# Optimization experiments

Hardware: AMD Instinct MI355X
Metric: run time of the kernel (lower is better)

The kernel has to match this reference:

```python
import jax, jax.numpy as jnp
import numpy as np


def setup_inputs() -> dict:
    key = jax.random.key(0)
    ks = jax.random.split(key, 7)
    B, D, H, M, E = 8192, 512, 512, 50, 3
    return {
        "x": jax.random.normal(ks[0], (B, D), dtype=jnp.float32),
        "mem": jax.random.normal(ks[1], (M, D), dtype=jnp.float32),
        "routing_logits": jax.random.normal(ks[2], (E,), dtype=jnp.float32),
        "proj_W": jax.random.normal(ks[3], (H, D), dtype=jnp.float32) * 0.02,
        "proj_b": jax.random.normal(ks[4], (H,), dtype=jnp.float32) * 0.02,
        "ops_W": jax.random.normal(ks[5], (E, H, H), dtype=jnp.float32) * 0.02,
        "ops_b": jax.random.normal(ks[6], (E, H), dtype=jnp.float32) * 0.02,
    }


def reference(x, mem, routing_logits, proj_W, proj_b, ops_W, ops_b):
    # novelty: mean over (batch, memory) of L2 distance between x rows and memory rows
    diff = x[:, None, :] - mem[None, :, :]                 # [B, M, D] -- dominant memory traffic
    novelty = jnp.minimum(1.5, jnp.mean(jnp.linalg.norm(diff, axis=-1)))

    # top-2 routing over softmax of the (per-module, input-independent) logits
    weights = jax.nn.softmax(routing_logits)
    _, top2 = jax.lax.top_k(weights, 2)
    idx_a, idx_b = top2[0], top2[1]

    # operator = ReLU -> Linear(H, H) -> ReLU (torch Linear: y = x @ W.T + b)
    def op(h, W, b):
        return jax.nn.relu(jnp.einsum("bh,oh->bo", jax.nn.relu(h), W) + b)

    x_proj = jnp.einsum("bd,hd->bh", x, proj_W) + proj_b   # [B, H]
    x1 = op(x_proj, ops_W[idx_a], ops_b[idx_a])
    out = op(x1, ops_W[idx_b], ops_b[idx_b])
    return out, novelty
```

## Files before the change

kernel.cpp:

```cpp
#include <hip/hip_runtime.h>
#include <hip/hip_bf16.h>

typedef _Float16 f16;
typedef _Float16 f16x8 __attribute__((ext_vector_type(8)));
typedef float f32x4 __attribute__((ext_vector_type(4)));

#define BD 512

__device__ __forceinline__ void llds16(const f16* g, f16* l) {
  __builtin_amdgcn_global_load_lds(
      (const __attribute__((address_space(1))) unsigned int*)g,
      (__attribute__((address_space(3))) unsigned int*)l,
      16, 0, 0);
}

__global__ __launch_bounds__(256) void conv_nov_w_kernel(
    const float* __restrict__ x, const float* __restrict__ memf,
    const float* __restrict__ projW, const float* __restrict__ opsW,
    f16* __restrict__ wh, f16* __restrict__ xh,
    float* __restrict__ novPart) {
  __shared__ __align__(16) f16 As[16 * BD];
  __shared__ float xn[16];
  __shared__ float red[4];
  const int t = threadIdx.x, l = t & 63, w = t >> 6;
  const int rbase = blockIdx.x * 16;

  {
    const int e = (blockIdx.x * 256 + t) * 8;
    const float* s = (e < 262144) ? (projW + e) : (opsW + (e - 262144));
    float4 v0 = ((const float4*)s)[0];
    float4 v1 = ((const float4*)s)[1];
    f16x8 h;
    h[0]=(f16)v0.x; h[1]=(f16)v0.y; h[2]=(f16)v0.z; h[3]=(f16)v0.w;
    h[4]=(f16)v1.x; h[5]=(f16)v1.y; h[6]=(f16)v1.z; h[7]=(f16)v1.w;
    *(f16x8*)&wh[e] = h;
  }

  #pragma unroll
  for (int rr = 0; rr < 4; ++rr) {
    const int r = w * 4 + rr;
    const float* src = x + (size_t)(rbase + r) * BD + l * 8;
    float4 v0 = *(const float4*)src;
    float4 v1 = *(const float4*)(src + 4);
    f16x8 h;
    h[0]=(f16)v0.x; h[1]=(f16)v0.y; h[2]=(f16)v0.z; h[3]=(f16)v0.w;
    h[4]=(f16)v1.x; h[5]=(f16)v1.y; h[6]=(f16)v1.z; h[7]=(f16)v1.w;
    *(f16x8*)&xh[(size_t)(rbase + r) * BD + l * 8] = h;
    const int cs = l ^ (r & 7);
    *(f16x8*)&As[r * BD + cs * 8] = h;
    float ss = v0.x*v0.x + v0.y*v0.y + v0.z*v0.z + v0.w*v0.w
             + v1.x*v1.x + v1.y*v1.y + v1.z*v1.z + v1.w*v1.w;
    #pragma unroll
    for (int off = 32; off; off >>= 1) ss += __shfl_down(ss, off, 64);
    if (l == 0) xn[r] = ss;
  }
  __syncthreads();

  const int lr = l & 15, lk = l >> 4;
  if (w < 4) {
    const int mm = w * 16 + lr;
    f32x4 acc = (f32x4){0.f, 0.f, 0.f, 0.f};
    float msq = 0.f;
    #pragma unroll
    for (int kk = 0; kk < BD; kk += 32) {
      f16x8 bfr;
      if (mm < 50) {
        const float* ms = memf + (size_t)mm * BD + kk + lk * 8;
        float4 v0 = ((const float4*)ms)[0];
        float4 v1 = ((const float4*)ms)[1];
        bfr[0]=(f16)v0.x; bfr[1]=(f16)v0.y; bfr[2]=(f16)v0.z; bfr[3]=(f16)v0.w;
        bfr[4]=(f16)v1.x; bfr[5]=(f16)v1.y; bfr[6]=(f16)v1.z; bfr[7]=(f16)v1.w;
        msq += v0.x*v0.x + v0.y*v0.y + v0.z*v0.z + v0.w*v0.w
             + v1.x*v1.x + v1.y*v1.y + v1.z*v1.z + v1.w*v1.w;
      } else {
        #pragma unroll
        for (int j = 0; j < 8; ++j) bfr[j] = (f16)0.f;
      }
      const int ch = (kk >> 3) + lk;
      f16x8 a = *(const f16x8*)&As[lr * BD + ((ch ^ (lr & 7)) << 3)];
      acc = __builtin_amdgcn_mfma_f32_16x16x32_f16(a, bfr, acc, 0, 0, 0);
    }
    msq += __shfl_xor(msq, 16, 64);
    msq += __shfl_xor(msq, 32, 64);
    float local = 0.f;
    if (mm < 50) {
      #pragma unroll
      for (int j = 0; j < 4; ++j) {
        const int r0 = lk * 4 + j;
        float d = xn[r0] - 2.f * acc[j] + msq;
        local += sqrtf(fmaxf(d, 0.f));
      }
    }
    #pragma unroll
    for (int off = 32; off; off >>= 1) local += __shfl_down(local, off, 64);
    if (l == 0) red[w] = local;
  }
  __syncthreads();
  if (t == 0) novPart[blockIdx.x] = red[0] + red[1] + red[2] + red[3];
}

template <int PICK, int OUTF16>
__global__ __launch_bounds__(256, 3) void gemm_relu_kernel(
    const f16* __restrict__ A, const f16* __restrict__ Wall,
    const float* __restrict__ ball, const float* __restrict__ logits,
    void* __restrict__ Out, const float* __restrict__ novPart,
    float* __restrict__ novOut) {
  __shared__ __align__(16) char lds[3 * 16384];

  const int t = threadIdx.x;
  const int l = t & 63;
  const int w = t >> 6;
  const int wr = w >> 1, wc = w & 1;
  const int lr = l & 15, lk = l >> 4;

  if (PICK == 0 && blockIdx.x == 0 && blockIdx.y == 0 && w == 0) {
    float s = 0.f;
    #pragma unroll
    for (int i = 0; i < 8; ++i) s += novPart[l + i * 64];
    #pragma unroll
    for (int off = 32; off; off >>= 1) s += __shfl_down(s, off, 64);
    if (l == 0) novOut[0] = fminf(1.5f, s * (1.0f / (8192.0f * 50.0f)));
  }

  int widx = 0;
  if (PICK > 0) {
    float l0 = logits[0], l1 = logits[1], l2 = logits[2];
    int ia = 0; float ba = l0;
    if (l1 > ba) { ba = l1; ia = 1; }
    if (l2 > ba) { ba = l2; ia = 2; }
    if (PICK == 1) {
      widx = ia;
    } else {
      int ib = 0; float bb2 = -3.4e38f;
      if (ia != 0)             { bb2 = l0; ib = 0; }
      if (ia != 1 && l1 > bb2) { bb2 = l1; ib = 1; }
      if (ia != 2 && l2 > bb2) { bb2 = l2; ib = 2; }
      widx = ib;
    }
  }
  const f16* W = Wall + (size_t)widx * BD * BD;
  const float* bias = ball + widx * BD;

  const int rowBase = blockIdx.x * 64;
  const int colBase = blockIdx.y * 64;

  f32x4 acc[2][2];
  #pragma unroll
  for (int m = 0; m < 2; ++m)
    #pragma unroll
    for (int n = 0; n < 2; ++n) acc[m][n] = (f32x4){0.f, 0.f, 0.f, 0.f};

  auto stage = [&](int buf, int kt) {
    f16* Ab = (f16*)(lds + buf * 16384);
    f16* Bb = (f16*)(lds + buf * 16384 + 8192);
    #pragma unroll
    for (int i = 0; i < 2; ++i) {
      const int o = i * 4096 + t * 16;
      const int row = o >> 7;
      const int sch = ((o >> 4) & 7) ^ (row & 7);
      llds16(A + (size_t)(rowBase + row) * BD + kt + sch * 8,
             Ab + (i * 4096 + w * 1024) / 2);
      llds16(W + (size_t)(colBase + row) * BD + kt + sch * 8,
             Bb + (i * 4096 + w * 1024) / 2);
    }
  };

  auto compute = [&](int buf) {
    const f16* Ab = (const f16*)(lds + buf * 16384);
    const f16* Bb = (const f16*)(lds + buf * 16384 + 8192);
    #pragma unroll
    for (int kk = 0; kk < 64; kk += 32) {
      const int ch = (kk >> 3) + lk;
      f16x8 af[2], bf[2];
      #pragma unroll
      for (int m = 0; m < 2; ++m) {
        const int row = wr * 32 + m * 16 + lr;
        af[m] = *(const f16x8*)&Ab[row * 64 + ((ch ^ (row & 7)) << 3)];
      }
      #pragma unroll
      for (int n = 0; n < 2; ++n) {
        const int row = wc * 32 + n * 16 + lr;
        bf[n] = *(const f16x8*)&Bb[row * 64 + ((ch ^ (row & 7)) << 3)];
      }
      __builtin_amdgcn_s_setprio(1);
      #pragma unroll
      for (int m = 0; m < 2; ++m)
        #pragma unroll
        for (int n = 0; n < 2; ++n)
          acc[m][n] = __builtin_amdgcn_mfma_f32_16x16x32_f16(af[m], bf[n], acc[m][n], 0, 0, 0);
      __builtin_amdgcn_s_setprio(0);
    }
  };

  stage(0, 0);
  stage(1, 64);
  #pragma unroll
  for (int t8 = 0; t8 < 8; ++t8) {
    if (t8 < 7) asm volatile("s_waitcnt vmcnt(4)" ::: "memory");
    else        asm volatile("s_waitcnt vmcnt(0)" ::: "memory");
    __builtin_amdgcn_s_barrier();
    if (t8 < 6) stage((t8 + 2) % 3, (t8 + 2) * 64);
    compute(t8 % 3);
    asm volatile("s_waitcnt lgkmcnt(0)" ::: "memory");
  }

  #pragma unroll
  for (int n = 0; n < 2; ++n) {
    const int col = colBase + wc * 32 + n * 16 + lr;
    const float bbv = bias[col];
    #pragma unroll
    for (int m = 0; m < 2; ++m) {
      #pragma unroll
      for (int j = 0; j < 4; ++j) {
        const int rowg = rowBase + wr * 32 + m * 16 + lk * 4 + j;
        float v = fmaxf(acc[m][n][j] + bbv, 0.f);
        if (OUTF16) ((f16*)Out)[(size_t)rowg * BD + col] = (f16)v;
        else        ((float*)Out)[(size_t)rowg * BD + col] = v;
      }
    }
  }
}

extern "C" void kernel_launch(void* const* d_in, const int* in_sizes, int n_in,
                              void* d_out, int out_size, void* d_ws, size_t ws_size,
                              hipStream_t stream) {
  const float* x      = (const float*)d_in[0];
  const float* memf   = (const float*)d_in[1];
  const float* logits = (const float*)d_in[2];
  const float* projW  = (const float*)d_in[3];
  const float* projB  = (const float*)d_in[4];
  const float* opsW   = (const float*)d_in[5];
  const float* opsB   = (const float*)d_in[6];
  float* out = (float*)d_out;

  char* ws = (char*)d_ws;
  f16*   xh      = (f16*)(ws);
  f16*   g0      = (f16*)(ws + 8388608);
  f16*   wh      = (f16*)(ws + 16777216);
  float* novPart = (float*)(ws + 18874368);

  conv_nov_w_kernel<<<512, 256, 0, stream>>>(x, memf, projW, opsW, wh, xh, novPart);

  gemm_relu_kernel<0, 1><<<dim3(128, 8), 256, 0, stream>>>(
      xh, wh, projB, logits, (void*)g0, novPart, out + 4194304);
  gemm_relu_kernel<1, 1><<<dim3(128, 8), 256, 0, stream>>>(
      g0, wh + 262144, opsB, logits, (void*)xh, novPart, out + 4194304);
  gemm_relu_kernel<2, 0><<<dim3(128, 8), 256, 0, stream>>>(
      xh, wh + 262144, opsB, logits, (void*)out, novPart, out + 4194304);
}
```

Measured before the change: 47.02 us.

## Stage memory rows in LDS as f16 and deepen GEMM pipeline to four buffers

The novelty kernel now loads all 50 memory rows once per block into LDS as swizzled f16, replacing per-wave global fp32 loads and conversions inside the K loop. The squared norm of each memory row is now computed from the f16 values, which slightly changes precision. The GEMM kernels move from a three-buffer to a four-buffer LDS ring, with three stages in flight and adjusted vmcnt waits, so that global-load latency is better hidden. In exchange, the larger LDS footprint (64KB per GEMM block, about 68KB for the novelty kernel) lowers occupancy bounds to 2 blocks per CU.

```diff
diff --git a/kernel.cpp b/kernel.cpp
--- a/kernel.cpp
+++ b/kernel.cpp
@@ -2,6 +2,7 @@
 #include <hip/hip_bf16.h>
 
 typedef _Float16 f16;
+typedef _Float16 f16x4 __attribute__((ext_vector_type(4)));
 typedef _Float16 f16x8 __attribute__((ext_vector_type(8)));
 typedef float f32x4 __attribute__((ext_vector_type(4)));
 
@@ -14,16 +15,29 @@
       16, 0, 0);
 }
 
-__global__ __launch_bounds__(256) void conv_nov_w_kernel(
+__global__ __launch_bounds__(256, 2) void conv_nov_w_kernel(
     const float* __restrict__ x, const float* __restrict__ memf,
     const float* __restrict__ projW, const float* __restrict__ opsW,
     f16* __restrict__ wh, f16* __restrict__ xh,
     float* __restrict__ novPart) {
+  __shared__ __align__(16) f16 memh[52 * BD];
   __shared__ __align__(16) f16 As[16 * BD];
   __shared__ float xn[16];
   __shared__ float red[4];
   const int t = threadIdx.x, l = t & 63, w = t >> 6;
   const int rbase = blockIdx.x * 16;
+
+  #pragma unroll
+  for (int i = 0; i < 25; ++i) {
+    const int idx = i * 256 + t;
+    const int row = idx >> 7;
+    const int c4  = idx & 127;
+    float4 v = ((const float4*)memf)[(size_t)row * 128 + c4];
+    f16x4 h;
+    h[0]=(f16)v.x; h[1]=(f16)v.y; h[2]=(f16)v.z; h[3]=(f16)v.w;
+    const int ch = c4 >> 1;
+    *(f16x4*)&memh[row * BD + (((ch ^ (row & 7)) << 3) | ((c4 & 1) << 2))] = h;
+  }
 
   {
     const int e = (blockIdx.x * 256 + t) * 8;
@@ -59,31 +73,28 @@
   const int lr = l & 15, lk = l >> 4;
   if (w < 4) {
     const int mm = w * 16 + lr;
+    const bool valid = (mm < 50);
     f32x4 acc = (f32x4){0.f, 0.f, 0.f, 0.f};
     float msq = 0.f;
     #pragma unroll
     for (int kk = 0; kk < BD; kk += 32) {
+      const int ch = (kk >> 3) + lk;
       f16x8 bfr;
-      if (mm < 50) {
-        const float* ms = memf + (size_t)mm * BD + kk + lk * 8;
-        float4 v0 = ((const float4*)ms)[0];
-        float4 v1 = ((const float4*)ms)[1];
-        bfr[0]=(f16)v0.x; bfr[1]=(f16)v0.y; bfr[2]=(f16)v0.z; bfr[3]=(f16)v0.w;
-        bfr[4]=(f16)v1.x; bfr[5]=(f16)v1.y; bfr[6]=(f16)v1.z; bfr[7]=(f16)v1.w;
-        msq += v0.x*v0.x + v0.y*v0.y + v0.z*v0.z + v0.w*v0.w
-             + v1.x*v1.x + v1.y*v1.y + v1.z*v1.z + v1.w*v1.w;
+      if (valid) {
+        bfr = *(const f16x8*)&memh[mm * BD + ((ch ^ (mm & 7)) << 3)];
+        #pragma unroll
+        for (int j = 0; j < 8; ++j) { float f = (float)bfr[j]; msq += f * f; }
       } else {
         #pragma unroll
         for (int j = 0; j < 8; ++j) bfr[j] = (f16)0.f;
       }
-      const int ch = (kk >> 3) + lk;
       f16x8 a = *(const f16x8*)&As[lr * BD + ((ch ^ (lr & 7)) << 3)];
       acc = __builtin_amdgcn_mfma_f32_16x16x32_f16(a, bfr, acc, 0, 0, 0);
     }
     msq += __shfl_xor(msq, 16, 64);
     msq += __shfl_xor(msq, 32, 64);
     float local = 0.f;
-    if (mm < 50) {
+    if (valid) {
       #pragma unroll
       for (int j = 0; j < 4; ++j) {
         const int r0 = lk * 4 + j;
@@ -100,12 +111,12 @@
 }
 
 template <int PICK, int OUTF16>
-__global__ __launch_bounds__(256, 3) void gemm_relu_kernel(
+__global__ __launch_bounds__(256, 2) void gemm_relu_kernel(
     const f16* __restrict__ A, const f16* __restrict__ Wall,
     const float* __restrict__ ball, const float* __restrict__ logits,
     void* __restrict__ Out, const float* __restrict__ novPart,
     float* __restrict__ novOut) {
-  __shared__ __align__(16) char lds[3 * 16384];
+  __shared__ __align__(16) char lds[4 * 16384];
 
   const int t = threadIdx.x;
   const int l = t & 63;
@@ -194,13 +205,15 @@
 
   stage(0, 0);
   stage(1, 64);
+  stage(2, 128);
   #pragma unroll
   for (int t8 = 0; t8 < 8; ++t8) {
-    if (t8 < 7) asm volatile("s_waitcnt vmcnt(4)" ::: "memory");
-    else        asm volatile("s_waitcnt vmcnt(0)" ::: "memory");
+    if (t8 < 6)       asm volatile("s_waitcnt vmcnt(8)" ::: "memory");
+    else if (t8 == 6) asm volatile("s_waitcnt vmcnt(4)" ::: "memory");
+    else              asm volatile("s_waitcnt vmcnt(0)" ::: "memory");
     __builtin_amdgcn_s_barrier();
-    if (t8 < 6) stage((t8 + 2) % 3, (t8 + 2) * 64);
-    compute(t8 % 3);
+    if (t8 < 5) stage((t8 + 3) & 3, (t8 + 3) * 64);
+    compute(t8 & 3);
     asm volatile("s_waitcnt lgkmcnt(0)" ::: "memory");
   }
 
```

Result: faster. 45.66 us (-2.9%).

## Fuse fp32-to-fp16 conversion and novelty computation into GEMM kernels

Applied to the files above, without the earlier changes.

Removes the separate conversion/novelty kernel. GEMMs now load fp32 x and weights directly through registers, convert them to fp16 and write them into LDS. The novelty distance is computed inside the first GEMM by blocks with by<2 before their main loop, and the final novelty reduction moves to the last GEMM. This saves one launch and the round trip of writing and reading fp16 copies. In exchange, weights are reconverted by every block, the LDS path now goes through registers instead of direct global-to-LDS loads, and the novelty blocks add imbalance to the first GEMM.

```diff
diff --git a/kernel.cpp b/kernel.cpp
--- a/kernel.cpp
+++ b/kernel.cpp
@@ -1,126 +1,48 @@
 #include <hip/hip_runtime.h>
-#include <hip/hip_bf16.h>
 
 typedef _Float16 f16;
 typedef _Float16 f16x8 __attribute__((ext_vector_type(8)));
 typedef float f32x4 __attribute__((ext_vector_type(4)));
 
 #define BD 512
-
-__device__ __forceinline__ void llds16(const f16* g, f16* l) {
-  __builtin_amdgcn_global_load_lds(
-      (const __attribute__((address_space(1))) unsigned int*)g,
-      (__attribute__((address_space(3))) unsigned int*)l,
-      16, 0, 0);
-}
-
-__global__ __launch_bounds__(256) void conv_nov_w_kernel(
-    const float* __restrict__ x, const float* __restrict__ memf,
-    const float* __restrict__ projW, const float* __restrict__ opsW,
-    f16* __restrict__ wh, f16* __restrict__ xh,
-    float* __restrict__ novPart) {
-  __shared__ __align__(16) f16 As[16 * BD];
-  __shared__ float xn[16];
+#define SBAR() __builtin_amdgcn_sched_barrier(0)
+
+__device__ __forceinline__ float4 gload16(const void* p) {
+  float4 r;
+  asm volatile("global_load_dwordx4 %0, %1, off" : "=v"(r) : "v"(p) : "memory");
+  return r;
+}
+__device__ __forceinline__ float gload4(const void* p) {
+  float r;
+  asm volatile("global_load_dword %0, %1, off" : "=v"(r) : "v"(p) : "memory");
+  return r;
+}
+__device__ __forceinline__ f16x8 cvt8(float4 a, float4 b) {
+  f16x8 h;
+  h[0]=(f16)a.x; h[1]=(f16)a.y; h[2]=(f16)a.z; h[3]=(f16)a.w;
+  h[4]=(f16)b.x; h[5]=(f16)b.y; h[6]=(f16)b.z; h[7]=(f16)b.w;
+  return h;
+}
+__device__ __forceinline__ float sq4(float4 v) {
+  return v.x*v.x + v.y*v.y + v.z*v.z + v.w*v.w;
+}
+
+template <int PICK, int OUTF16>
+__global__ __launch_bounds__(256, 2) void gemm_fused_kernel(
+    const void* __restrict__ Asrc, const float* __restrict__ Wsrc,
+    const float* __restrict__ memf, const float* __restrict__ ball,
+    const float* __restrict__ logits, void* __restrict__ Out,
+    float* __restrict__ novPart, float* __restrict__ novOut) {
+  __shared__ __align__(16) char lds[32768];
+  __shared__ float xn[64];
+  __shared__ float mn[32];
   __shared__ float red[4];
+
   const int t = threadIdx.x, l = t & 63, w = t >> 6;
-  const int rbase = blockIdx.x * 16;
-
-  {
-    const int e = (blockIdx.x * 256 + t) * 8;
-    const float* s = (e < 262144) ? (projW + e) : (opsW + (e - 262144));
-    float4 v0 = ((const float4*)s)[0];
-    float4 v1 = ((const float4*)s)[1];
-    f16x8 h;
-    h[0]=(f16)v0.x; h[1]=(f16)v0.y; h[2]=(f16)v0.z; h[3]=(f16)v0.w;
-    h[4]=(f16)v1.x; h[5]=(f16)v1.y; h[6]=(f16)v1.z; h[7]=(f16)v1.w;
-    *(f16x8*)&wh[e] = h;
-  }
-
-  #pragma unroll
-  for (int rr = 0; rr < 4; ++rr) {
-    const int r = w * 4 + rr;
-    const float* src = x + (size_t)(rbase + r) * BD + l * 8;
-    float4 v0 = *(const float4*)src;
-    float4 v1 = *(const float4*)(src + 4);
-    f16x8 h;
-    h[0]=(f16)v0.x; h[1]=(f16)v0.y; h[2]=(f16)v0.z; h[3]=(f16)v0.w;
-    h[4]=(f16)v1.x; h[5]=(f16)v1.y; h[6]=(f16)v1.z; h[7]=(f16)v1.w;
-    *(f16x8*)&xh[(size_t)(rbase + r) * BD + l * 8] = h;
-    const int cs = l ^ (r & 7);
-    *(f16x8*)&As[r * BD + cs * 8] = h;
-    float ss = v0.x*v0.x + v0.y*v0.y + v0.z*v0.z + v0.w*v0.w
-             + v1.x*v1.x + v1.y*v1.y + v1.z*v1.z + v1.w*v1.w;
-    #pragma unroll
-    for (int off = 32; off; off >>= 1) ss += __shfl_down(ss, off, 64);
-    if (l == 0) xn[r] = ss;
-  }
-  __syncthreads();
-
-  const int lr = l & 15, lk = l >> 4;
-  if (w < 4) {
-    const int mm = w * 16 + lr;
-    f32x4 acc = (f32x4){0.f, 0.f, 0.f, 0.f};
-    float msq = 0.f;
-    #pragma unroll
-    for (int kk = 0; kk < BD; kk += 32) {
-      f16x8 bfr;
-      if (mm < 50) {
-        const float* ms = memf + (size_t)mm * BD + kk + lk * 8;
-        float4 v0 = ((const float4*)ms)[0];
-        float4 v1 = ((const float4*)ms)[1];
-        bfr[0]=(f16)v0.x; bfr[1]=(f16)v0.y; bfr[2]=(f16)v0.z; bfr[3]=(f16)v0.w;
-        bfr[4]=(f16)v1.x; bfr[5]=(f16)v1.y; bfr[6]=(f16)v1.z; bfr[7]=(f16)v1.w;
-        msq += v0.x*v0.x + v0.y*v0.y + v0.z*v0.z + v0.w*v0.w
-             + v1.x*v1.x + v1.y*v1.y + v1.z*v1.z + v1.w*v1.w;
-      } else {
-        #pragma unroll
-        for (int j = 0; j < 8; ++j) bfr[j] = (f16)0.f;
-      }
-      const int ch = (kk >> 3) + lk;
-      f16x8 a = *(const f16x8*)&As[lr * BD + ((ch ^ (lr & 7)) << 3)];
-      acc = __builtin_amdgcn_mfma_f32_16x16x32_f16(a, bfr, acc, 0, 0, 0);
-    }
-    msq += __shfl_xor(msq, 16, 64);
-    msq += __shfl_xor(msq, 32, 64);
-    float local = 0.f;
-    if (mm < 50) {
-      #pragma unroll
-      for (int j = 0; j < 4; ++j) {
-        const int r0 = lk * 4 + j;
-        float d = xn[r0] - 2.f * acc[j] + msq;
-        local += sqrtf(fmaxf(d, 0.f));
-      }
-    }
-    #pragma unroll
-    for (int off = 32; off; off >>= 1) local += __shfl_down(local, off, 64);
-    if (l == 0) red[w] = local;
-  }
-  __syncthreads();
-  if (t == 0) novPart[blockIdx.x] = red[0] + red[1] + red[2] + red[3];
-}
-
-template <int PICK, int OUTF16>
-__global__ __launch_bounds__(256, 3) void gemm_relu_kernel(
-    const f16* __restrict__ A, const f16* __restrict__ Wall,
-    const float* __restrict__ ball, const float* __restrict__ logits,
-    void* __restrict__ Out, const float* __restrict__ novPart,
-    float* __restrict__ novOut) {
-  __shared__ __align__(16) char lds[3 * 16384];
-
-  const int t = threadIdx.x;
-  const int l = t & 63;
-  const int w = t >> 6;
   const int wr = w >> 1, wc = w & 1;
   const int lr = l & 15, lk = l >> 4;
-
-  if (PICK == 0 && blockIdx.x == 0 && blockIdx.y == 0 && w == 0) {
-    float s = 0.f;
-    #pragma unroll
-    for (int i = 0; i < 8; ++i) s += novPart[l + i * 64];
-    #pragma unroll
-    for (int off = 32; off; off >>= 1) s += __shfl_down(s, off, 64);
-    if (l == 0) novOut[0] = fminf(1.5f, s * (1.0f / (8192.0f * 50.0f)));
-  }
+  const int bx = blockIdx.x, by = blockIdx.y;
+  const int rowBase = bx * 64, colBase = by * 64;
 
   int widx = 0;
   if (PICK > 0) {
@@ -138,11 +60,137 @@
       widx = ib;
     }
   }
-  const f16* W = Wall + (size_t)widx * BD * BD;
+  const float* Wf = Wsrc + (size_t)widx * 262144;
   const float* bias = ball + widx * BD;
 
-  const int rowBase = blockIdx.x * 64;
-  const int colBase = blockIdx.y * 64;
+  float bbv[2];
+  bbv[0] = gload4(&bias[colBase + wc * 32 + lr]);
+  bbv[1] = gload4(&bias[colBase + wc * 32 + 16 + lr]);
+
+  if (PICK == 2 && bx == 0 && by == 0 && w == 0) {
+    float s = novPart[l] + novPart[l + 64] + novPart[l + 128] + novPart[l + 192];
+    #pragma unroll
+    for (int off = 32; off; off >>= 1) s += __shfl_down(s, off, 64);
+    if (l == 0) novOut[0] = fminf(1.5f, s * (1.0f / (8192.0f * 50.0f)));
+  }
+  asm volatile("s_waitcnt vmcnt(0)" ::: "memory");
+  SBAR();
+
+  if (PICK == 0 && by < 2) {
+    const float* xf = (const float*)Asrc;
+    const int xrow = t >> 2;
+    const int xc0 = (t * 2) & 7;
+    const int mrow = t >> 3;
+    const int mch = t & 7;
+    const int mglob = by * 32 + mrow;
+    const int msrcRow = (mglob < 50) ? mglob : 49;
+    const bool mvalid = (mglob < 50);
+
+    float4 rx[2][4], rm[2][2];
+    f32x4 nacc0 = (f32x4){0.f,0.f,0.f,0.f};
+    f32x4 nacc1 = (f32x4){0.f,0.f,0.f,0.f};
+    float xsq = 0.f, msq = 0.f;
+
+    auto novIssue = [&](int slot, int cc) {
+      const float* xs = xf + (size_t)(rowBase + xrow) * BD + cc * 64 + xc0 * 8;
+      rx[slot][0] = gload16(xs);      rx[slot][1] = gload16(xs + 4);
+      rx[slot][2] = gload16(xs + 8);  rx[slot][3] = gload16(xs + 12);
+      const float* ms = memf + (size_t)msrcRow * BD + cc * 64 + mch * 8;
+      rm[slot][0] = gload16(ms);      rm[slot][1] = gload16(ms + 4);
+    };
+
+    novIssue(0, 0);
+    novIssue(1, 1);
+    #pragma unroll
+    for (int cc = 0; cc < 8; ++cc) {
+      if (cc < 7) asm volatile("s_waitcnt vmcnt(6)" ::: "memory");
+      else        asm volatile("s_waitcnt vmcnt(0)" ::: "memory");
+      SBAR();
+      const int sl = cc & 1;
+      f16* XC = (f16*)(lds + sl * 12288);
+      f16* MC = (f16*)(lds + sl * 12288 + 8192);
+      xsq += sq4(rx[sl][0]) + sq4(rx[sl][1]) + sq4(rx[sl][2]) + sq4(rx[sl][3]);
+      *(f16x8*)&XC[xrow * 64 + ((xc0 ^ (xrow & 7)) << 3)]       = cvt8(rx[sl][0], rx[sl][1]);
+      *(f16x8*)&XC[xrow * 64 + (((xc0 + 1) ^ (xrow & 7)) << 3)] = cvt8(rx[sl][2], rx[sl][3]);
+      f16x8 mh = cvt8(rm[sl][0], rm[sl][1]);
+      if (mvalid) {
+        msq += sq4(rm[sl][0]) + sq4(rm[sl][1]);
+      } else {
+        #pragma unroll
+        for (int j = 0; j < 8; ++j) mh[j] = (f16)0.f;
+      }
+      *(f16x8*)&MC[mrow * 64 + ((mch ^ (mrow & 7)) << 3)] = mh;
+      asm volatile("s_waitcnt lgkmcnt(0)" ::: "memory");
+      SBAR();
+      __builtin_amdgcn_s_barrier();
+      if (cc + 2 < 8) novIssue(sl, cc + 2);
+      #pragma unroll
+      for (int kk = 0; kk < 64; kk += 32) {
+        const int ch = (kk >> 3) + lk;
+        const int ar = w * 16 + lr;
+        f16x8 af = *(const f16x8*)&XC[ar * 64 + ((ch ^ (ar & 7)) << 3)];
+        const int br0 = lr;
+        f16x8 bf0 = *(const f16x8*)&MC[br0 * 64 + ((ch ^ (br0 & 7)) << 3)];
+        nacc0 = __builtin_amdgcn_mfma_f32_16x16x32_f16(af, bf0, nacc0, 0, 0, 0);
+        const int br1 = 16 + lr;
+        f16x8 bf1 = *(const f16x8*)&MC[br1 * 64 + ((ch ^ (br1 & 7)) << 3)];
+        nacc1 = __builtin_amdgcn_mfma_f32_16x16x32_f16(af, bf1, nacc1, 0, 0, 0);
+      }
+    }
+    xsq += __shfl_xor(xsq, 1, 64); xsq += __shfl_xor(xsq, 2, 64);
+    if ((l & 3) == 0) xn[t >> 2] = xsq;
+    msq += __shfl_xor(msq, 1, 64); msq += __shfl_xor(msq, 2, 64); msq += __shfl_xor(msq, 4, 64);
+    if ((l & 7) == 0) mn[t >> 3] = msq;
+    __syncthreads();
+    float local = 0.f;
+    {
+      const int m0 = by * 32 + lr;
+      if (m0 < 50) {
+        #pragma unroll
+        for (int j = 0; j < 4; ++j) {
+          const int row = w * 16 + lk * 4 + j;
+          float d = xn[row] - 2.f * nacc0[j] + mn[lr];
+          local += sqrtf(fmaxf(d, 0.f));
+        }
+      }
+      const int m1 = by * 32 + 16 + lr;
+      if (m1 < 50) {
+        #pragma unroll
+        for (int j = 0; j < 4; ++j) {
+          const int row = w * 16 + lk * 4 + j;
+          float d = xn[row] - 2.f * nacc1[j] + mn[16 + lr];
+          local += sqrtf(fmaxf(d, 0.f));
+        }
+      }
+    }
+    #pragma unroll
+    for (int off = 32; off; off >>= 1) local += __shfl_down(local, off, 64);
+    if (l == 0) red[w] = local;
+    __syncthreads();
+    if (t == 0) novPart[by * 128 + bx] = red[0] + red[1] + red[2] + red[3];
+    __syncthreads();
+    asm volatile("s_waitcnt vmcnt(0)" ::: "memory");
+    SBAR();
+  }
+
+  const int arow = t >> 2;
+  const int ac0 = (t * 2) & 7;
+  float4 ra[2][4], rb[2][4];
+
+  auto issue = [&](int slot, int tt) {
+    const int kt = tt * 64;
+    if constexpr (PICK == 0) {
+      const float* as = (const float*)Asrc + (size_t)(rowBase + arow) * BD + kt + ac0 * 8;
+      ra[slot][0] = gload16(as);      ra[slot][1] = gload16(as + 4);
+      ra[slot][2] = gload16(as + 8);  ra[slot][3] = gload16(as + 12);
+    } else {
+      const f16* as = (const f16*)Asrc + (size_t)(rowBase + arow) * BD + kt + ac0 * 8;
+      ra[slot][0] = gload16(as);      ra[slot][1] = gload16(as + 8);
+    }
+    const float* bs = Wf + (size_t)(colBase + arow) * BD + kt + ac0 * 8;
+    rb[slot][0] = gload16(bs);      rb[slot][1] = gload16(bs + 4);
+    rb[slot][2] = gload16(bs + 8);  rb[slot][3] = gload16(bs + 12);
+  };
 
   f32x4 acc[2][2];
   #pragma unroll
@@ -150,24 +198,33 @@
     #pragma unroll
     for (int n = 0; n < 2; ++n) acc[m][n] = (f32x4){0.f, 0.f, 0.f, 0.f};
 
-  auto stage = [&](int buf, int kt) {
-    f16* Ab = (f16*)(lds + buf * 16384);
-    f16* Bb = (f16*)(lds + buf * 16384 + 8192);
-    #pragma unroll
-    for (int i = 0; i < 2; ++i) {
-      const int o = i * 4096 + t * 16;
-      const int row = o >> 7;
-      const int sch = ((o >> 4) & 7) ^ (row & 7);
-      llds16(A + (size_t)(rowBase + row) * BD + kt + sch * 8,
-             Ab + (i * 4096 + w * 1024) / 2);
-      llds16(W + (size_t)(colBase + row) * BD + kt + sch * 8,
-             Bb + (i * 4096 + w * 1024) / 2);
-    }
-  };
-
-  auto compute = [&](int buf) {
-    const f16* Ab = (const f16*)(lds + buf * 16384);
-    const f16* Bb = (const f16*)(lds + buf * 16384 + 8192);
+  issue(0, 0);
+  issue(1, 1);
+  #pragma unroll
+  for (int t8 = 0; t8 < 8; ++t8) {
+    if (t8 < 7) {
+      if constexpr (PICK == 0) asm volatile("s_waitcnt vmcnt(8)" ::: "memory");
+      else                     asm volatile("s_waitcnt vmcnt(6)" ::: "memory");
+    } else {
+      asm volatile("s_waitcnt vmcnt(0)" ::: "memory");
+    }
+    SBAR();
+    const int sl = t8 & 1;
+    f16* Ab = (f16*)(lds + sl * 16384);
+    f16* Bb = (f16*)(lds + sl * 16384 + 8192);
+    if constexpr (PICK == 0) {
+      *(f16x8*)&Ab[arow * 64 + ((ac0 ^ (arow & 7)) << 3)]       = cvt8(ra[sl][0], ra[sl][1]);
+      *(f16x8*)&Ab[arow * 64 + (((ac0 + 1) ^ (arow & 7)) << 3)] = cvt8(ra[sl][2], ra[sl][3]);
+    } else {
+      *(f16x8*)&Ab[arow * 64 + ((ac0 ^ (arow & 7)) << 3)]       = *(f16x8*)&ra[sl][0];
+      *(f16x8*)&Ab[arow * 64 + (((ac0 + 1) ^ (arow & 7)) << 3)] = *(f16x8*)&ra[sl][1];
+    }
+    *(f16x8*)&Bb[arow * 64 + ((ac0 ^ (arow & 7)) << 3)]       = cvt8(rb[sl][0], rb[sl][1]);
+    *(f16x8*)&Bb[arow * 64 + (((ac0 + 1) ^ (arow & 7)) << 3)] = cvt8(rb[sl][2], rb[sl][3]);
+    asm volatile("s_waitcnt lgkmcnt(0)" ::: "memory");
+    SBAR();
+    __builtin_amdgcn_s_barrier();
+    if (t8 + 2 < 8) issue(sl, t8 + 2);
     #pragma unroll
     for (int kk = 0; kk < 64; kk += 32) {
       const int ch = (kk >> 3) + lk;
@@ -190,30 +247,17 @@
           acc[m][n] = __builtin_amdgcn_mfma_f32_16x16x32_f16(af[m], bf[n], acc[m][n], 0, 0, 0);
       __builtin_amdgcn_s_setprio(0);
     }
-  };
-
-  stage(0, 0);
-  stage(1, 64);
-  #pragma unroll
-  for (int t8 = 0; t8 < 8; ++t8) {
-    if (t8 < 7) asm volatile("s_waitcnt vmcnt(4)" ::: "memory");
-    else        asm volatile("s_waitcnt vmcnt(0)" ::: "memory");
-    __builtin_amdgcn_s_barrier();
-    if (t8 < 6) stage((t8 + 2) % 3, (t8 + 2) * 64);
-    compute(t8 % 3);
-    asm volatile("s_waitcnt lgkmcnt(0)" ::: "memory");
   }
 
   #pragma unroll
   for (int n = 0; n < 2; ++n) {
     const int col = colBase + wc * 32 + n * 16 + lr;
-    const float bbv = bias[col];
     #pragma unroll
     for (int m = 0; m < 2; ++m) {
       #pragma unroll
       for (int j = 0; j < 4; ++j) {
         const int rowg = rowBase + wr * 32 + m * 16 + lk * 4 + j;
-        float v = fmaxf(acc[m][n][j] + bbv, 0.f);
+        float v = fmaxf(acc[m][n][j] + bbv[n], 0.f);
         if (OUTF16) ((f16*)Out)[(size_t)rowg * BD + col] = (f16)v;
         else        ((float*)Out)[(size_t)rowg * BD + col] = v;
       }
@@ -234,17 +278,14 @@
   float* out = (float*)d_out;
 
   char* ws = (char*)d_ws;
-  f16*   xh      = (f16*)(ws);
-  f16*   g0      = (f16*)(ws + 8388608);
-  f16*   wh      = (f16*)(ws + 16777216);
-  float* novPart = (float*)(ws + 18874368);
-
-  conv_nov_w_kernel<<<512, 256, 0, stream>>>(x, memf, projW, opsW, wh, xh, novPart);
-
-  gemm_relu_kernel<0, 1><<<dim3(128, 8), 256, 0, stream>>>(
-      xh, wh, projB, logits, (void*)g0, novPart, out + 4194304);
-  gemm_relu_kernel<1, 1><<<dim3(128, 8), 256, 0, stream>>>(
-      g0, wh + 262144, opsB, logits, (void*)xh, novPart, out + 4194304);
-  gemm_relu_kernel<2, 0><<<dim3(128, 8), 256, 0, stream>>>(
-      xh, wh + 262144, opsB, logits, (void*)out, novPart, out + 4194304);
-}
+  f16*   g0      = (f16*)(ws);
+  f16*   h1      = (f16*)(ws + 8388608);
+  float* novPart = (float*)(ws + 16777216);
+
+  gemm_fused_kernel<0, 1><<<dim3(128, 8), 256, 0, stream>>>(
+      (const void*)x, projW, memf, projB, logits, (void*)g0, novPart, out + 4194304);
+  gemm_fused_kernel<1, 1><<<dim3(128, 8), 256, 0, stream>>>(
+      (const void*)g0, opsW, memf, opsB, logits, (void*)h1, novPart, out + 4194304);
+  gemm_fused_kernel<2, 0><<<dim3(128, 8), 256, 0, stream>>>(
+      (const void*)h1, opsW, memf, opsB, logits, (void*)out, novPart, out + 4194304);
+}
```

After: 62.33 us. 32.6% more time.
